# Optimization experiments

Measured on AMD Instinct MI355X. Metric: run time of the kernel, lower is better.

The kernel has to match this reference:

```python
import jax, jax.numpy as jnp
import numpy as np

NX, NF = 8192, 8192
F_SIZE, OUT_SIZE, D_ATT = 512, 256, 128
N_GRAPHS = 16
NEG_INF = -1e9


def setup_inputs() -> dict:
    key = jax.random.key(0)
    ks = jax.random.split(key, 10)
    f = jax.random.normal(ks[0], (NF, F_SIZE), dtype=jnp.float32)
    x = jax.random.normal(ks[1], (NX, OUT_SIZE), dtype=jnp.float32)
    h = jax.random.normal(ks[2], (NX, OUT_SIZE), dtype=jnp.float32)
    edge_index = jax.random.randint(ks[3], (2, NX), 0, NX)
    edge_type = jax.random.randint(ks[4], (NX,), 0, 4)
    f_batch = jnp.sort(jax.random.randint(ks[5], (NF,), 0, N_GRAPHS))
    x_batch = jnp.sort(jax.random.randint(ks[6], (NX,), 0, N_GRAPHS))
    x_init = jax.random.normal(ks[7], (NX, OUT_SIZE), dtype=jnp.float32)
    # Glorot-initialized projection weights, stored [in, out]
    def glorot(k, shape):
        lim = np.sqrt(6.0 / (shape[0] + shape[1]))
        return jax.random.uniform(k, shape, jnp.float32, -lim, lim)
    W_h = glorot(ks[8], (OUT_SIZE, D_ATT))
    kk, kv = jax.random.split(ks[9])
    W_key = glorot(kk, (F_SIZE, D_ATT))
    W_value = glorot(kv, (F_SIZE, OUT_SIZE))
    return {"f": f, "x": x, "h": h, "edge_index": edge_index,
            "edge_type": edge_type, "f_batch": f_batch, "x_batch": x_batch,
            "x_init": x_init, "W_h": W_h, "W_key": W_key, "W_value": W_value}


def reference(f, x, h, edge_index, edge_type, f_batch, x_batch, x_init,
              W_h, W_key, W_value):
    # QKV projections (bias-free linears)
    query = h @ W_h          # [Nx, 128]
    key = f @ W_key          # [Nf, 128]
    value = f @ W_value      # [Nf, out_size]
    # Block-diagonal batch mask: attend only within the same graph
    not_same = x_batch[:, None] != f_batch[None, :]       # [Nx, Nf]
    scores = jnp.einsum('qd,kd->qk', query, key)          # [Nx, Nf]
    scores = jnp.where(not_same, NEG_INF, scores)
    attn = jax.nn.softmax(scores, axis=-1)
    context = attn @ value                                 # [Nx, out_size]
    return context, attn
```

## Files before the change

### kernel.cpp

```cpp
#include <hip/hip_runtime.h>

#define NX_  8192
#define NF_  8192
#define DQ_  128
#define OUT_ 256
#define FS_  512

typedef float  f32x4  __attribute__((ext_vector_type(4)));
typedef short  bf16x8 __attribute__((ext_vector_type(8)));

static __device__ __forceinline__ void nt_store4(const float4& w, float* p) {
  f32x4 v; v.x = w.x; v.y = w.y; v.z = w.z; v.w = w.w;
  __builtin_nontemporal_store(v, (f32x4*)p);
}
static __device__ __forceinline__ ushort f2bf(float f) {
  union { float f; uint u; } c; c.f = f;
  uint r = c.u + 0x7FFF + ((c.u >> 16) & 1);
  return (ushort)(r >> 16);
}
static __device__ __forceinline__ float bf2f(ushort u) {
  union { uint u; float f; } c; c.u = ((uint)u) << 16; return c.f;
}

__global__ void ranges_kernel(const int* __restrict__ xb, const int* __restrict__ fb,
                              int* __restrict__ rng) {
  int t = threadIdx.x;
  if (t < 17) {
    int lo = 0, hi = NX_;
    while (lo < hi) { int mid = (lo + hi) >> 1; if (xb[mid] < t) lo = mid + 1; else hi = mid; }
    rng[t] = lo;
  } else if (t < 34) {
    int g = t - 17;
    int lo = 0, hi = NF_;
    while (lo < hi) { int mid = (lo + hi) >> 1; if (fb[mid] < g) lo = mid + 1; else hi = mid; }
    rng[17 + g] = lo;
  }
}

__global__ __launch_bounds__(256) void wprep_kernel(const float* __restrict__ Wh,
                                                    const float* __restrict__ Wk,
                                                    const float* __restrict__ Wv,
                                                    ushort* __restrict__ WhTh, ushort* __restrict__ WhTl,
                                                    ushort* __restrict__ WkTh, ushort* __restrict__ WkTl,
                                                    ushort* __restrict__ WvTh, ushort* __restrict__ WvTl) {
  int idx = blockIdx.x * 256 + threadIdx.x;
  float w; ushort* ph; ushort* pl; int off;
  if (idx < 32768) {
    int n = idx >> 8, k = idx & 255;
    w = Wh[k * DQ_ + n]; ph = WhTh; pl = WhTl; off = idx;
  } else if (idx < 98304) {
    int i = idx - 32768; int n = i >> 9, k = i & 511;
    w = Wk[k * DQ_ + n]; ph = WkTh; pl = WkTl; off = i;
  } else if (idx < 229376) {
    int i = idx - 98304; int n = i >> 9, k = i & 511;
    w = Wv[k * OUT_ + n]; ph = WvTh; pl = WvTl; off = i;
  } else return;
  ushort hi = f2bf(w);
  ph[off] = hi;
  pl[off] = f2bf(w - bf2f(hi));
}

__global__ __launch_bounds__(256) void prep_split(const float* __restrict__ f,
                                                  const float* __restrict__ h,
                                                  ushort* __restrict__ fh, ushort* __restrict__ fl,
                                                  ushort* __restrict__ hh, ushort* __restrict__ hl) {
  const int NF4 = (NF_ * FS_) / 4;
  const int NH4 = (NX_ * OUT_) / 4;
  int stride = gridDim.x * 256;
  for (int i = blockIdx.x * 256 + threadIdx.x; i < NF4 + NH4; i += stride) {
    const float4* src; ushort* ph; ushort* pl; int j;
    if (i < NF4) { src = (const float4*)f; ph = fh; pl = fl; j = i; }
    else         { src = (const float4*)h; ph = hh; pl = hl; j = i - NF4; }
    float4 v = src[j];
    ushort4 uh, ul;
    uh.x = f2bf(v.x); ul.x = f2bf(v.x - bf2f(uh.x));
    uh.y = f2bf(v.y); ul.y = f2bf(v.y - bf2f(uh.y));
    uh.z = f2bf(v.z); ul.z = f2bf(v.z - bf2f(uh.z));
    uh.w = f2bf(v.w); ul.w = f2bf(v.w - bf2f(uh.w));
    ((ushort4*)ph)[j] = uh;
    ((ushort4*)pl)[j] = ul;
  }
}

__global__ __launch_bounds__(256) void gemm_all(const ushort* __restrict__ fh, const ushort* __restrict__ fl,
                                                const ushort* __restrict__ hh, const ushort* __restrict__ hl,
                                                const ushort* __restrict__ WhTh, const ushort* __restrict__ WhTl,
                                                const ushort* __restrict__ WkTh, const ushort* __restrict__ WkTl,
                                                const ushort* __restrict__ WvTh, const ushort* __restrict__ WvTl,
                                                ushort* __restrict__ Qh, ushort* __restrict__ Ql,
                                                ushort* __restrict__ Kh, ushort* __restrict__ Kl,
                                                ushort* __restrict__ VT) {
  __shared__ ushort Ahi[64][64], Alo[64][64];
  __shared__ ushort Bhi[64][64], Blo[64][64];
  int bid = blockIdx.x;
  const ushort *Ah, *Al, *BTh, *BTl;
  int N, K, lid, mode;
  if (bid < 256)      { Ah = hh; Al = hl; BTh = WhTh; BTl = WhTl; N = DQ_;  K = OUT_; mode = 0; lid = bid; }
  else if (bid < 512) { Ah = fh; Al = fl; BTh = WkTh; BTl = WkTl; N = DQ_;  K = FS_;  mode = 1; lid = bid - 256; }
  else                { Ah = fh; Al = fl; BTh = WvTh; BTl = WvTl; N = OUT_; K = FS_;  mode = 2; lid = bid - 512; }
  int nbn = N >> 6;
  int bm = (lid / nbn) << 6, bn = (lid % nbn) << 6;
  int tid = threadIdx.x, lane = tid & 63, w = tid >> 6;
  int srow = tid >> 2, skq = (tid & 3) << 4;
  f32x4 acc[4];
#pragma unroll
  for (int i = 0; i < 4; ++i) acc[i] = (f32x4){0.f, 0.f, 0.f, 0.f};

  for (int k0 = 0; k0 < K; k0 += 64) {
    size_t aoff = (size_t)(bm + srow) * K + k0 + skq;
    size_t boff = (size_t)(bn + srow) * K + k0 + skq;
#pragma unroll
    for (int j = 0; j < 2; ++j) {
      int sk = (skq + (j << 3)) ^ ((srow & 7) << 3);
      *(uint4*)&Ahi[srow][sk] = *(const uint4*)(Ah + aoff + (j << 3));
      *(uint4*)&Alo[srow][sk] = *(const uint4*)(Al + aoff + (j << 3));
      *(uint4*)&Bhi[srow][sk] = *(const uint4*)(BTh + boff + (j << 3));
      *(uint4*)&Blo[srow][sk] = *(const uint4*)(BTl + boff + (j << 3));
    }
    __syncthreads();
#pragma unroll
    for (int step = 0; step < 2; ++step) {
      int kb = (step << 5) + ((lane >> 4) << 3);
      int brow = (w << 4) + (lane & 15);
      int bsk = kb ^ ((brow & 7) << 3);
      bf16x8 bh = *(const bf16x8*)&Bhi[brow][bsk];
      bf16x8 bl = *(const bf16x8*)&Blo[brow][bsk];
#pragma unroll
      for (int i = 0; i < 4; ++i) {
        int ar = (i << 4) + (lane & 15);
        int ask = kb ^ ((ar & 7) << 3);
        bf16x8 ah = *(const bf16x8*)&Ahi[ar][ask];
        bf16x8 al = *(const bf16x8*)&Alo[ar][ask];
        acc[i] = __builtin_amdgcn_mfma_f32_16x16x32_bf16(ah, bh, acc[i], 0, 0, 0);
        acc[i] = __builtin_amdgcn_mfma_f32_16x16x32_bf16(al, bh, acc[i], 0, 0, 0);
        acc[i] = __builtin_amdgcn_mfma_f32_16x16x32_bf16(ah, bl, acc[i], 0, 0, 0);
      }
    }
    __syncthreads();
  }
  int cr = (lane >> 4) << 2, cc = lane & 15;
  if (mode < 2) {
    ushort* Ch = (mode == 0) ? Qh : Kh;
    ushort* Cl = (mode == 0) ? Ql : Kl;
#pragma unroll
    for (int i = 0; i < 4; ++i)
#pragma unroll
      for (int r = 0; r < 4; ++r) {
        float v = acc[i][r];
        ushort hi = f2bf(v);
        size_t o = (size_t)(bm + (i << 4) + cr + r) * DQ_ + bn + (w << 4) + cc;
        Ch[o] = hi;
        Cl[o] = f2bf(v - bf2f(hi));
      }
  } else {
#pragma unroll
    for (int i = 0; i < 4; ++i)
#pragma unroll
      for (int r = 0; r < 4; ++r)
        VT[(size_t)(bn + (w << 4) + cc) * NX_ + bm + (i << 4) + cr + r] = f2bf(acc[i][r]);
  }
}

__global__ __launch_bounds__(256) void fused_attn(const ushort* __restrict__ Qh, const ushort* __restrict__ Ql,
                                                  const ushort* __restrict__ Kh, const ushort* __restrict__ Kl,
                                                  const ushort* __restrict__ VT,
                                                  const int* __restrict__ xb,
                                                  const int* __restrict__ rng,
                                                  float* __restrict__ attn,
                                                  float* __restrict__ ctx) {
  __shared__ ushort Pb[16][784];
  __shared__ float wred[8][16];
  int r0 = blockIdx.x << 4;
  int tid = threadIdx.x;
  int w = tid >> 6, lane = tid & 63;
  int lg = lane >> 4, li = lane & 15;
  int g0 = xb[r0], g1 = xb[r0 + 15];
  for (int g = g0; g <= g1; ++g) {
    int rs = rng[g], re = rng[g + 1];
    int ars = (rs > r0 ? rs : r0) - r0;
    int are = (re < r0 + 16 ? re : r0 + 16) - r0;
    if (ars >= are) continue;
    int ks = rng[17 + g], ke = rng[18 + g];
    int kbase = ks & ~7;
    const ushort* qrh = Qh + (size_t)(r0 + li) * DQ_ + (lg << 3);
    const ushort* qrl = Ql + (size_t)(r0 + li) * DQ_ + (lg << 3);
    bf16x8 qh[4], ql[4];
#pragma unroll
    for (int db = 0; db < 4; ++db) {
      qh[db] = *(const bf16x8*)(qrh + (db << 5));
      ql[db] = *(const bf16x8*)(qrl + (db << 5));
    }
    f32x4 s[12];
#pragma unroll
    for (int tt = 0; tt < 12; ++tt) {
      int key0 = kbase + (((tt << 2) + w) << 4);
      int krow = key0 + li; if (krow > NF_ - 1) krow = NF_ - 1;
      const ushort* krh = Kh + (size_t)krow * DQ_ + (lg << 3);
      const ushort* krl = Kl + (size_t)krow * DQ_ + (lg << 3);
      f32x4 a = (f32x4){0.f, 0.f, 0.f, 0.f};
#pragma unroll
      for (int db = 0; db < 4; ++db) {
        bf16x8 kh = *(const bf16x8*)(krh + (db << 5));
        bf16x8 kl = *(const bf16x8*)(krl + (db << 5));
        a = __builtin_amdgcn_mfma_f32_16x16x32_bf16(qh[db], kh, a, 0, 0, 0);
        a = __builtin_amdgcn_mfma_f32_16x16x32_bf16(ql[db], kh, a, 0, 0, 0);
        a = __builtin_amdgcn_mfma_f32_16x16x32_bf16(qh[db], kl, a, 0, 0, 0);
      }
      s[tt] = a;
    }
    float pm[4];
#pragma unroll
    for (int r = 0; r < 4; ++r) pm[r] = -3.0e38f;
#pragma unroll
    for (int tt = 0; tt < 12; ++tt) {
      int col = kbase + (((tt << 2) + w) << 4) + li;
      bool valid = (col >= ks) && (col < ke);
#pragma unroll
      for (int r = 0; r < 4; ++r) pm[r] = fmaxf(pm[r], valid ? s[tt][r] : -3.0e38f);
    }
#pragma unroll
    for (int r = 0; r < 4; ++r) {
      pm[r] = fmaxf(pm[r], __shfl_xor(pm[r], 1));
      pm[r] = fmaxf(pm[r], __shfl_xor(pm[r], 2));
      pm[r] = fmaxf(pm[r], __shfl_xor(pm[r], 4));
      pm[r] = fmaxf(pm[r], __shfl_xor(pm[r], 8));
    }
    if (li == 0) {
#pragma unroll
      for (int r = 0; r < 4; ++r) wred[w][(lg << 2) + r] = pm[r];
    }
    __syncthreads();
    float m[4], ps[4];
#pragma unroll
    for (int r = 0; r < 4; ++r) {
      int row = (lg << 2) + r;
      m[r] = fmaxf(fmaxf(wred[0][row], wred[1][row]), fmaxf(wred[2][row], wred[3][row]));
      ps[r] = 0.f;
    }
#pragma unroll
    for (int tt = 0; tt < 12; ++tt) {
      int col = kbase + (((tt << 2) + w) << 4) + li;
      bool valid = (col >= ks) && (col < ke);
#pragma unroll
      for (int r = 0; r < 4; ++r) {
        float e = valid ? __expf(s[tt][r] - m[r]) : 0.f;
        s[tt][r] = e;
        ps[r] += e;
      }
    }
#pragma unroll
    for (int r = 0; r < 4; ++r) {
      ps[r] += __shfl_xor(ps[r], 1);
      ps[r] += __shfl_xor(ps[r], 2);
      ps[r] += __shfl_xor(ps[r], 4);
      ps[r] += __shfl_xor(ps[r], 8);
    }
    if (li == 0) {
#pragma unroll
      for (int r = 0; r < 4; ++r) wred[4 + w][(lg << 2) + r] = ps[r];
    }
    __syncthreads();
    float inv[4];
#pragma unroll
    for (int r = 0; r < 4; ++r) {
      int row = (lg << 2) + r;
      inv[r] = 1.0f / (wred[4][row] + wred[5][row] + wred[6][row] + wred[7][row]);
    }
#pragma unroll
    for (int tt = 0; tt < 12; ++tt) {
      int kc = (((tt << 2) + w) << 4) + li;
#pragma unroll
      for (int r = 0; r < 4; ++r)
        Pb[(lg << 2) + r][kc] = f2bf(s[tt][r] * inv[r]);
    }
    __syncthreads();
    for (int idx = tid; idx < 16 * (NF_ / 4); idx += 256) {
      int row = idx >> 11;
      if (row < ars || row >= are) continue;
      int col = (idx & 2047) << 2;
      float4 wv = make_float4(0.f, 0.f, 0.f, 0.f);
      int rel = col - kbase;
      if (rel >= 0 && rel < 768) {
        ushort4 pu = *(const ushort4*)&Pb[row][rel];
        wv.x = bf2f(pu.x); wv.y = bf2f(pu.y); wv.z = bf2f(pu.z); wv.w = bf2f(pu.w);
      }
      nt_store4(wv, attn + (size_t)(r0 + row) * NF_ + col);
    }
    int nsteps = (ke - kbase + 31) >> 5;
    f32x4 pacc[4];
#pragma unroll
    for (int ot = 0; ot < 4; ++ot) pacc[ot] = (f32x4){0.f, 0.f, 0.f, 0.f};
    for (int st = 0; st < nsteps; ++st) {
      bf16x8 pfr = *(const bf16x8*)&Pb[li][(st << 5) + (lg << 3)];
      int kaddr = kbase + (st << 5) + (lg << 3);
      if (kaddr > NF_ - 8) kaddr = NF_ - 8;
#pragma unroll
      for (int ot = 0; ot < 4; ++ot) {
        const ushort* vr = VT + (size_t)((w << 6) + (ot << 4) + li) * NX_ + kaddr;
        bf16x8 vfr = *(const bf16x8*)vr;
        pacc[ot] = __builtin_amdgcn_mfma_f32_16x16x32_bf16(pfr, vfr, pacc[ot], 0, 0, 0);
      }
    }
#pragma unroll
    for (int ot = 0; ot < 4; ++ot)
#pragma unroll
      for (int r = 0; r < 4; ++r) {
        int row = (lg << 2) + r;
        if (row >= ars && row < are)
          ctx[(size_t)(r0 + row) * OUT_ + (w << 6) + (ot << 4) + li] = pacc[ot][r];
      }
    __syncthreads();
  }
}

extern "C" void kernel_launch(void* const* d_in, const int* in_sizes, int n_in,
                              void* d_out, int out_size, void* d_ws, size_t ws_size,
                              hipStream_t stream) {
  const float* f   = (const float*)d_in[0];
  const float* h   = (const float*)d_in[2];
  const int*   fb  = (const int*)d_in[5];
  const int*   xbt = (const int*)d_in[6];
  const float* Wh  = (const float*)d_in[8];
  const float* Wk  = (const float*)d_in[9];
  const float* Wv  = (const float*)d_in[10];

  float* ctx_out  = (float*)d_out;
  float* attn_out = ctx_out + (size_t)NX_ * OUT_;

  ushort* fh   = (ushort*)d_ws;
  ushort* fl   = fh + (size_t)NF_ * FS_;
  ushort* hh   = fl + (size_t)NF_ * FS_;
  ushort* hl   = hh + (size_t)NX_ * OUT_;
  ushort* Qh   = hl + (size_t)NX_ * OUT_;
  ushort* Ql   = Qh + (size_t)NX_ * DQ_;
  ushort* Kh   = Ql + (size_t)NX_ * DQ_;
  ushort* Kl   = Kh + (size_t)NF_ * DQ_;
  ushort* VT   = Kl + (size_t)NF_ * DQ_;
  ushort* WhTh = VT + (size_t)OUT_ * NX_;
  ushort* WhTl = WhTh + 32768;
  ushort* WkTh = WhTl + 32768;
  ushort* WkTl = WkTh + 65536;
  ushort* WvTh = WkTl + 65536;
  ushort* WvTl = WvTh + 131072;
  int*    rng  = (int*)(WvTl + 131072);

  hipLaunchKernelGGL(ranges_kernel, dim3(1), dim3(64), 0, stream, xbt, fb, rng);
  hipLaunchKernelGGL(wprep_kernel, dim3(896), dim3(256), 0, stream,
                     Wh, Wk, Wv, WhTh, WhTl, WkTh, WkTl, WvTh, WvTl);
  hipLaunchKernelGGL(prep_split, dim3(2048), dim3(256), 0, stream,
                     f, h, fh, fl, hh, hl);
  hipLaunchKernelGGL(gemm_all, dim3(1024), dim3(256), 0, stream,
                     fh, fl, hh, hl, WhTh, WhTl, WkTh, WkTl, WvTh, WvTl,
                     Qh, Ql, Kh, Kl, VT);
  hipLaunchKernelGGL(fused_attn, dim3(NX_ / 16), dim3(256), 0, stream,
                     Qh, Ql, Kh, Kl, VT, xbt, rng, attn_out, ctx_out);
}
```

Measured before the change: 420.1 us.

## Zero attention matrix upfront, write only in-graph tiles, drop V split-precision

A new kernel zero-fills the whole 256MB attention output with nontemporal stores. The fused attention kernel then writes only the block-diagonal window per graph instead of sweeping every column of each row with mostly zeros. The value GEMM drops the hi/lo split passes, since V is stored in bf16 anyway, and it writes VT with packed ushort4 stores. Total memory traffic for the zeros stays the same, but it moves to a simpler bandwidth-bound pass, which cuts scattered per-graph overhead and loop work in the attention kernel.

```diff
diff --git a/kernel.cpp b/kernel.cpp
--- a/kernel.cpp
+++ b/kernel.cpp
@@ -35,6 +35,14 @@
     while (lo < hi) { int mid = (lo + hi) >> 1; if (fb[mid] < g) lo = mid + 1; else hi = mid; }
     rng[17 + g] = lo;
   }
+}
+
+__global__ __launch_bounds__(256) void zero_attn(float* __restrict__ attn) {
+  const size_t n4 = (size_t)NX_ * NF_ / 4;
+  size_t stride = (size_t)gridDim.x * 256;
+  float4 z = make_float4(0.f, 0.f, 0.f, 0.f);
+  for (size_t i = (size_t)blockIdx.x * 256 + threadIdx.x; i < n4; i += stride)
+    nt_store4(z, attn + (i << 2));
 }
 
 __global__ __launch_bounds__(256) void wprep_kernel(const float* __restrict__ Wh,
@@ -86,7 +94,7 @@
                                                 const ushort* __restrict__ hh, const ushort* __restrict__ hl,
                                                 const ushort* __restrict__ WhTh, const ushort* __restrict__ WhTl,
                                                 const ushort* __restrict__ WkTh, const ushort* __restrict__ WkTl,
-                                                const ushort* __restrict__ WvTh, const ushort* __restrict__ WvTl,
+                                                const ushort* __restrict__ WvTh,
                                                 ushort* __restrict__ Qh, ushort* __restrict__ Ql,
                                                 ushort* __restrict__ Kh, ushort* __restrict__ Kl,
                                                 ushort* __restrict__ VT) {
@@ -97,11 +105,12 @@
   int N, K, lid, mode;
   if (bid < 256)      { Ah = hh; Al = hl; BTh = WhTh; BTl = WhTl; N = DQ_;  K = OUT_; mode = 0; lid = bid; }
   else if (bid < 512) { Ah = fh; Al = fl; BTh = WkTh; BTl = WkTl; N = DQ_;  K = FS_;  mode = 1; lid = bid - 256; }
-  else                { Ah = fh; Al = fl; BTh = WvTh; BTl = WvTl; N = OUT_; K = FS_;  mode = 2; lid = bid - 512; }
+  else                { Ah = fh; Al = fh; BTh = WvTh; BTl = WvTh; N = OUT_; K = FS_;  mode = 2; lid = bid - 512; }
   int nbn = N >> 6;
   int bm = (lid / nbn) << 6, bn = (lid % nbn) << 6;
   int tid = threadIdx.x, lane = tid & 63, w = tid >> 6;
   int srow = tid >> 2, skq = (tid & 3) << 4;
+  bool split = (mode < 2);
   f32x4 acc[4];
 #pragma unroll
   for (int i = 0; i < 4; ++i) acc[i] = (f32x4){0.f, 0.f, 0.f, 0.f};
@@ -113,9 +122,11 @@
     for (int j = 0; j < 2; ++j) {
       int sk = (skq + (j << 3)) ^ ((srow & 7) << 3);
       *(uint4*)&Ahi[srow][sk] = *(const uint4*)(Ah + aoff + (j << 3));
-      *(uint4*)&Alo[srow][sk] = *(const uint4*)(Al + aoff + (j << 3));
       *(uint4*)&Bhi[srow][sk] = *(const uint4*)(BTh + boff + (j << 3));
-      *(uint4*)&Blo[srow][sk] = *(const uint4*)(BTl + boff + (j << 3));
+      if (split) {
+        *(uint4*)&Alo[srow][sk] = *(const uint4*)(Al + aoff + (j << 3));
+        *(uint4*)&Blo[srow][sk] = *(const uint4*)(BTl + boff + (j << 3));
+      }
     }
     __syncthreads();
 #pragma unroll
@@ -124,16 +135,18 @@
       int brow = (w << 4) + (lane & 15);
       int bsk = kb ^ ((brow & 7) << 3);
       bf16x8 bh = *(const bf16x8*)&Bhi[brow][bsk];
-      bf16x8 bl = *(const bf16x8*)&Blo[brow][bsk];
 #pragma unroll
       for (int i = 0; i < 4; ++i) {
         int ar = (i << 4) + (lane & 15);
         int ask = kb ^ ((ar & 7) << 3);
         bf16x8 ah = *(const bf16x8*)&Ahi[ar][ask];
-        bf16x8 al = *(const bf16x8*)&Alo[ar][ask];
         acc[i] = __builtin_amdgcn_mfma_f32_16x16x32_bf16(ah, bh, acc[i], 0, 0, 0);
-        acc[i] = __builtin_amdgcn_mfma_f32_16x16x32_bf16(al, bh, acc[i], 0, 0, 0);
-        acc[i] = __builtin_amdgcn_mfma_f32_16x16x32_bf16(ah, bl, acc[i], 0, 0, 0);
+        if (split) {
+          bf16x8 bl = *(const bf16x8*)&Blo[brow][bsk];
+          bf16x8 al = *(const bf16x8*)&Alo[ar][ask];
+          acc[i] = __builtin_amdgcn_mfma_f32_16x16x32_bf16(al, bh, acc[i], 0, 0, 0);
+          acc[i] = __builtin_amdgcn_mfma_f32_16x16x32_bf16(ah, bl, acc[i], 0, 0, 0);
+        }
       }
     }
     __syncthreads();
@@ -154,10 +167,12 @@
       }
   } else {
 #pragma unroll
-    for (int i = 0; i < 4; ++i)
-#pragma unroll
-      for (int r = 0; r < 4; ++r)
-        VT[(size_t)(bn + (w << 4) + cc) * NX_ + bm + (i << 4) + cr + r] = f2bf(acc[i][r]);
+    for (int i = 0; i < 4; ++i) {
+      ushort4 o;
+      o.x = f2bf(acc[i][0]); o.y = f2bf(acc[i][1]);
+      o.z = f2bf(acc[i][2]); o.w = f2bf(acc[i][3]);
+      *(ushort4*)&VT[(size_t)(bn + (w << 4) + cc) * NX_ + bm + (i << 4) + cr] = o;
+    }
   }
 }
 
@@ -274,16 +289,15 @@
         Pb[(lg << 2) + r][kc] = f2bf(s[tt][r] * inv[r]);
     }
     __syncthreads();
-    for (int idx = tid; idx < 16 * (NF_ / 4); idx += 256) {
-      int row = idx >> 11;
+    for (int idx = tid; idx < 16 * 192; idx += 256) {
+      int row = idx / 192;
       if (row < ars || row >= are) continue;
-      int col = (idx & 2047) << 2;
-      float4 wv = make_float4(0.f, 0.f, 0.f, 0.f);
-      int rel = col - kbase;
-      if (rel >= 0 && rel < 768) {
-        ushort4 pu = *(const ushort4*)&Pb[row][rel];
-        wv.x = bf2f(pu.x); wv.y = bf2f(pu.y); wv.z = bf2f(pu.z); wv.w = bf2f(pu.w);
-      }
+      int c4 = idx - row * 192;
+      int col = kbase + (c4 << 2);
+      if (col >= NF_) continue;
+      ushort4 pu = *(const ushort4*)&Pb[row][c4 << 2];
+      float4 wv;
+      wv.x = bf2f(pu.x); wv.y = bf2f(pu.y); wv.z = bf2f(pu.z); wv.w = bf2f(pu.w);
       nt_store4(wv, attn + (size_t)(r0 + row) * NF_ + col);
     }
     int nsteps = (ke - kbase + 31) >> 5;
@@ -345,12 +359,13 @@
   int*    rng  = (int*)(WvTl + 131072);
 
   hipLaunchKernelGGL(ranges_kernel, dim3(1), dim3(64), 0, stream, xbt, fb, rng);
+  hipLaunchKernelGGL(zero_attn, dim3(4096), dim3(256), 0, stream, attn_out);
   hipLaunchKernelGGL(wprep_kernel, dim3(896), dim3(256), 0, stream,
                      Wh, Wk, Wv, WhTh, WhTl, WkTh, WkTl, WvTh, WvTl);
   hipLaunchKernelGGL(prep_split, dim3(2048), dim3(256), 0, stream,
                      f, h, fh, fl, hh, hl);
   hipLaunchKernelGGL(gemm_all, dim3(1024), dim3(256), 0, stream,
-                     fh, fl, hh, hl, WhTh, WhTl, WkTh, WkTl, WvTh, WvTl,
+                     fh, fl, hh, hl, WhTh, WhTl, WkTh, WkTl, WvTh,
                      Qh, Ql, Kh, Kl, VT);
   hipLaunchKernelGGL(fused_attn, dim3(NX_ / 16), dim3(256), 0, stream,
                      Qh, Ql, Kh, Kl, VT, xbt, rng, attn_out, ctx_out);
```

New measurement: 445.0 us. 5.9% more time.
